# Kernel tuning notes

Measured on AMD Instinct MI355X. Metric: run time of the kernel, lower is better.

Reference implementation:

```python
import jax, jax.numpy as jnp
import numpy as np

# MORR all-pass ring parameters (MORRConfig_20um defaults: attenuation / self-coupling)
A_MORR = 0.8578
R_MORR = 0.8578
KS = 3       # kernel_size
MB = 8       # miniblock (circulant block size)
BN_EPS = 1e-5


def mrr_roundtrip_phase_to_tr(phi):
    # through-port transmission of an all-pass microring vs roundtrip phase
    c = jnp.cos(phi)
    num = A_MORR * A_MORR - 2.0 * A_MORR * R_MORR * c + R_MORR * R_MORR
    den = 1.0 - 2.0 * A_MORR * R_MORR * c + (A_MORR * R_MORR) ** 2
    return num / den


def setup_inputs() -> dict:
    key = jax.random.key(0)
    k1, k2 = jax.random.split(key, 2)
    B, C, H, W = 64, 64, 32, 32
    outC = 64
    q = (C * KS * KS + MB - 1) // MB   # grid_dim_x = 72
    p = (outC + MB - 1) // MB          # grid_dim_y = 8
    x = jax.random.normal(k1, (B, C, H, W), jnp.float32)
    weight = jax.random.normal(k2, (p, q, MB), jnp.float32) * 0.05  # circulant eigen-vectors per block
    gamma = jnp.ones((outC,), jnp.float32)   # BatchNorm2d weight
    beta = jnp.zeros((outC,), jnp.float32)   # BatchNorm2d bias
    return {"x": x, "weight": weight, "gamma": gamma, "beta": beta}


def reference(x, weight, gamma, beta):
    B, C, H, W = x.shape
    p, q, mb = weight.shape
    outC = gamma.shape[0]
    Ho, Wo = H, W  # stride=1, padding=1, ks=3
    L = Ho * Wo
    # im2col (torch F.unfold ordering: C major, then kh, kw)
    xp = jnp.pad(x, ((0, 0), (0, 0), (1, 1), (1, 1)))
    cols = jnp.stack([xp[:, :, i:i + Ho, j:j + Wo]
                      for i in range(KS) for j in range(KS)], axis=2)  # [B,C,9,Ho,Wo]
    cols = cols.reshape(B, C * KS * KS, L).transpose(0, 2, 1)          # [B,L,C*k*k]
    assert C * KS * KS == q * mb, "patch dim must pad to q*mb"
    s = cols.reshape(B, L, q, mb)
    s = s * s  # optical intensity (power) fed into the MORR
    # block-circulant weight: Wc[p,q,i,j] = weight[p,q,(i-j) mod mb]
    i_idx = jnp.arange(mb)
    idx = (i_idx[:, None] - i_idx[None, :]) % mb
    Wc = weight[:, :, idx]                                             # [p,q,mb,mb]
    # accumulated roundtrip phase per output node
    phase = jnp.einsum('blqj,pqij->blpi', s, Wc)                       # [B,L,p,mb]
    tr = mrr_roundtrip_phase_to_tr(phase)
    out = tr.reshape(B, L, p * mb)[:, :, :outC]                        # truncate to out_channel
    out = out.transpose(0, 2, 1).reshape(B, outC, Ho, Wo)
    # BatchNorm2d (training mode: batch statistics) + Hardtanh(-1, 1)
    mean = out.mean(axis=(0, 2, 3), keepdims=True)
    var = out.var(axis=(0, 2, 3), keepdims=True)
    y = (out - mean) * jax.lax.rsqrt(var + BN_EPS)
    y = y * gamma[None, :, None, None] + beta[None, :, None, None]
    return jnp.clip(y, -1.0, 1.0)
```

## Files before the change

### kernel.cpp

```cpp
#include <hip/hip_runtime.h>


#define A_MORR 0.8578f
#define R_MORR 0.8578f
#define TR_C1 (A_MORR * A_MORR + R_MORR * R_MORR)
#define TR_C2 (-2.0f * A_MORR * R_MORR)
#define TR_C3 (1.0f + (A_MORR * R_MORR) * (A_MORR * R_MORR))
#define BN_EPS 1e-5f

#define NPIX 65536
#define X2_LO 17408
#define SMEM_BYTES 34816
#define NBLK 1024

typedef __attribute__((ext_vector_type(8))) short bf16x8;
typedef __attribute__((ext_vector_type(16))) float f32x16;

__device__ __forceinline__ void bf16split(float s, unsigned short& h, unsigned short& l) {
    union { float f; unsigned u; } cv; cv.f = s;
    unsigned r = (cv.u + 0x7fffu + ((cv.u >> 16) & 1u)) & 0xffff0000u;
    h = (unsigned short)(r >> 16);
    union { unsigned u; float f; } hv; hv.u = r;
    float lo = s - hv.f;
    cv.f = lo;
    unsigned r2 = cv.u + 0x7fffu + ((cv.u >> 16) & 1u);
    l = (unsigned short)(r2 >> 16);
}

__global__ __launch_bounds__(256) void prep_kernel(const float* __restrict__ w,
                                                   char* __restrict__ wfrag) {
    int gtid = blockIdx.x * 256 + threadIdx.x;
    if (gtid < 36864) {
        int j    = gtid & 7;
        int lane = (gtid >> 3) & 63;
        int okm  = gtid >> 9;
        int mt   = okm & 1;
        int ks   = (okm >> 1) & 3;
        int off  = okm >> 3;
        int oc   = mt * 32 + (lane & 31);
        int c    = ks * 16 + (lane >> 5) * 8 + j;
        int kg   = c * 9 + off;
        float val = w[(oc >> 3) * 576 + (kg >> 3) * 8 + ((oc - kg) & 7)];
        unsigned short h, l;
        bf16split(val, h, l);
        ((unsigned short*)(wfrag + okm * 2048))[lane * 8 + j] = h;
        ((unsigned short*)(wfrag + okm * 2048 + 1024))[lane * 8 + j] = l;
    }
}

__global__ __launch_bounds__(256, 4) void conv_kernel(const float* __restrict__ x,
                                                      const char* __restrict__ wfrag,
                                                      float* __restrict__ out,
                                                      float* __restrict__ partials) {
    const int rt  = blockIdx.x;
    const int b   = blockIdx.y;
    const int bid = b * 16 + rt;
    const int tid = threadIdx.x;

    const int lane = tid & 63;
    const int wv   = tid >> 6;
    const int wmt  = wv & 1;
    const int kh   = wv >> 1;
    const int col  = lane & 31;
    const int hs   = lane >> 5;

    __shared__ __align__(16) char smem[SMEM_BYTES];

    if (tid < 128) {
        int pr = tid & 1;
        int q  = (tid >> 1) & 7;
        int rc = tid >> 4;
        int r  = rc >> 1;
        int cc = (rc & 1) ? 33 : 0;
        int g  = q ^ (cc & 7);
        *(uint4*)(smem + pr * X2_LO + ((r * 34 + cc) << 7) + (g << 4)) = uint4{0, 0, 0, 0};
    }

    {
        const int co = tid & 31;
        const int qg = tid >> 5;
        const int c  = 1 + co;
        const int gw = (qg ^ (c & 7)) << 4;
        const float* xb = x + (size_t)(b * 64 + qg * 8) * 1024 + co;
#pragma unroll
        for (int r = 0; r < 4; ++r) {
            int gr = rt * 2 - 1 + r;
            float v[8];
#pragma unroll
            for (int j = 0; j < 8; ++j) v[j] = 0.0f;
            if (gr >= 0 && gr < 32) {
#pragma unroll
                for (int j = 0; j < 8; ++j) v[j] = xb[j * 1024 + gr * 32];
            }
            unsigned hp[4], lp[4];
#pragma unroll
            for (int p = 0; p < 4; ++p) {
                unsigned short h0, l0, h1, l1;
                float s0 = v[2 * p] * v[2 * p];
                float s1 = v[2 * p + 1] * v[2 * p + 1];
                bf16split(s0, h0, l0);
                bf16split(s1, h1, l1);
                hp[p] = (unsigned)h0 | ((unsigned)h1 << 16);
                lp[p] = (unsigned)l0 | ((unsigned)l1 << 16);
            }
            char* dst = smem + ((r * 34 + c) << 7) + gw;
            *(uint4*)dst            = uint4{hp[0], hp[1], hp[2], hp[3]};
            *(uint4*)(dst + X2_LO)  = uint4{lp[0], lp[1], lp[2], lp[3]};
        }
    }
    __syncthreads();

    f32x16 acc0, acc1;
#pragma unroll
    for (int i = 0; i < 16; ++i) { acc0[i] = 0.f; acc1[i] = 0.f; }

    const char* wbase = wfrag + wmt * 2048 + (size_t)lane * 16;

#pragma unroll
    for (int dj = 0; dj < 3; ++dj) {
        const int c2 = col + dj;
        const int c7 = c2 & 7;
#pragma unroll
        for (int ksi = 0; ksi < 2; ++ksi) {
            const int ks = kh * 2 + ksi;
            const int gg = ((ks * 2 + hs) ^ c7) << 4;
            bf16x8 bh[4], bl[4];
#pragma unroll
            for (int rr = 0; rr < 4; ++rr) {
                const char* sp = smem + ((rr * 34 + c2) << 7) + gg;
                bh[rr] = *(const bf16x8*)sp;
                bl[rr] = *(const bf16x8*)(sp + X2_LO);
            }
#pragma unroll
            for (int di = 0; di < 3; ++di) {
                const char* wp = wbase + (di * 3 + dj) * 16384 + ks * 4096;
                bf16x8 ah = *(const bf16x8*)wp;
                bf16x8 al = *(const bf16x8*)(wp + 1024);
                acc0 = __builtin_amdgcn_mfma_f32_32x32x16_bf16(ah, bh[di],     acc0, 0, 0, 0);
                acc1 = __builtin_amdgcn_mfma_f32_32x32x16_bf16(ah, bh[di + 1], acc1, 0, 0, 0);
                acc0 = __builtin_amdgcn_mfma_f32_32x32x16_bf16(ah, bl[di],     acc0, 0, 0, 0);
                acc1 = __builtin_amdgcn_mfma_f32_32x32x16_bf16(ah, bl[di + 1], acc1, 0, 0, 0);
                acc0 = __builtin_amdgcn_mfma_f32_32x32x16_bf16(al, bh[di],     acc0, 0, 0, 0);
                acc1 = __builtin_amdgcn_mfma_f32_32x32x16_bf16(al, bh[di + 1], acc1, 0, 0, 0);
            }
        }
    }

    float* mg = (float*)smem;
    __syncthreads();
    {
        const int wslot = wmt * 2 + kh;
        if (kh == 0) {
#pragma unroll
            for (int j = 0; j < 16; ++j) mg[(wslot * 16 + j) * 64 + lane] = acc1[j];
        } else {
#pragma unroll
            for (int j = 0; j < 16; ++j) mg[(wslot * 16 + j) * 64 + lane] = acc0[j];
        }
    }
    __syncthreads();
    f32x16 phi;
    {
        const int rslot = wmt * 2 + (kh ^ 1);
        if (kh == 0) {
#pragma unroll
            for (int j = 0; j < 16; ++j) phi[j] = acc0[j] + mg[(rslot * 16 + j) * 64 + lane];
        } else {
#pragma unroll
            for (int j = 0; j < 16; ++j) phi[j] = acc1[j] + mg[(rslot * 16 + j) * 64 + lane];
        }
    }

    float tv[16];
    {
        const size_t obase = ((size_t)b * 64 + wmt * 32) * 1024 + (rt * 2 + kh) * 32 + col;
#pragma unroll
        for (int j = 0; j < 16; ++j) {
            float cp = __cosf(phi[j]);
            float t  = fmaf(TR_C2, cp, TR_C1) / fmaf(TR_C2, cp, TR_C3);
            tv[j] = t;
            int ocl = (j & 3) + 8 * (j >> 2) + 4 * hs;
            out[obase + (size_t)ocl * 1024] = t;
        }
    }

    float* red1 = (float*)smem;
    float* red2 = red1 + 64 * 66;
    __syncthreads();
#pragma unroll
    for (int j = 0; j < 16; ++j) {
        int ocl = (j & 3) + 8 * (j >> 2) + 4 * hs;
        int ri  = (wmt * 32 + ocl) * 66 + kh * 33 + col;
        red1[ri] = tv[j];
        red2[ri] = tv[j] * tv[j];
    }
    __syncthreads();
    if (tid < 64) {
        float s1 = 0.f, s2 = 0.f;
#pragma unroll
        for (int k = 0; k < 64; ++k) {
            int idx = tid * 66 + (k >> 5) * 33 + (k & 31);
            s1 += red1[idx];
            s2 += red2[idx];
        }
        partials[(size_t)tid * NBLK + bid]        = s1;
        partials[(size_t)(64 + tid) * NBLK + bid] = s2;
    }
}

__global__ __launch_bounds__(512) void stats_kernel(const float* __restrict__ partials,
                                                    const float* __restrict__ gamma,
                                                    const float* __restrict__ beta,
                                                    float* __restrict__ ss) {
    const int c   = blockIdx.x;
    const int tid = threadIdx.x;
    __shared__ float r1[512], r2[512];
    r1[tid] = partials[(size_t)c * NBLK + tid] + partials[(size_t)c * NBLK + 512 + tid];
    r2[tid] = partials[(size_t)(64 + c) * NBLK + tid]
            + partials[(size_t)(64 + c) * NBLK + 512 + tid];
    __syncthreads();
#pragma unroll
    for (int s = 256; s > 0; s >>= 1) {
        if (tid < s) {
            r1[tid] += r1[tid + s];
            r2[tid] += r2[tid + s];
        }
        __syncthreads();
    }
    if (tid == 0) {
        const float invN = 1.0f / (float)NPIX;
        float mean = r1[0] * invN;
        float var  = r2[0] * invN - mean * mean;
        float sc   = gamma[c] * rsqrtf(var + BN_EPS);
        ss[c]      = sc;
        ss[64 + c] = beta[c] - mean * sc;
    }
}

__global__ __launch_bounds__(256) void norm_kernel(float* __restrict__ out,
                                                   const float* __restrict__ ss) {
    int i = blockIdx.x * 256 + threadIdx.x;
    float4 v = ((float4*)out)[i];
    int oc = (i >> 8) & 63;
    float sc = ss[oc];
    float sh = ss[64 + oc];
    v.x = fminf(1.0f, fmaxf(-1.0f, fmaf(v.x, sc, sh)));
    v.y = fminf(1.0f, fmaxf(-1.0f, fmaf(v.y, sc, sh)));
    v.z = fminf(1.0f, fmaxf(-1.0f, fmaf(v.z, sc, sh)));
    v.w = fminf(1.0f, fmaxf(-1.0f, fmaf(v.w, sc, sh)));
    ((float4*)out)[i] = v;
}

extern "C" void kernel_launch(void* const* d_in, const int* in_sizes, int n_in,
                              void* d_out, int out_size, void* d_ws, size_t ws_size,
                              hipStream_t stream) {
    const float* x     = (const float*)d_in[0];
    const float* w     = (const float*)d_in[1];
    const float* gamma = (const float*)d_in[2];
    const float* beta  = (const float*)d_in[3];
    float* out = (float*)d_out;

    char*  wfrag    = (char*)d_ws;
    float* partials = (float*)((char*)d_ws + 147456);
    float* ss       = partials + 128 * NBLK;

    hipLaunchKernelGGL(prep_kernel, dim3(144), dim3(256), 0, stream, w, wfrag);
    hipLaunchKernelGGL(conv_kernel, dim3(16, 64), dim3(256), 0, stream, x, wfrag, out, partials);
    hipLaunchKernelGGL(stats_kernel, dim3(64), dim3(512), 0, stream, partials, gamma, beta, ss);
    hipLaunchKernelGGL(norm_kernel, dim3(4096), dim3(256), 0, stream, out, ss);
}
```

Measured before the change: 41.24 us.

## Fuse BN stats and normalization into conv kernel via cooperative grid sync

Turns the conv kernel into a cooperative launch. After writing per-block partial sums it does a grid-wide sync, lets 64 blocks reduce the per-channel statistics, syncs the grid again, and then applies the BN affine transform and clamp in registers before one store of the output. This removes the separate stats and norm kernel launches and the extra read-modify-write pass over the 16 MB output. In exchange it adds two grid barriers, requires all 1024 blocks to be co-resident (256 CUs × 4), and keeps the old three-kernel path as a fallback when occupancy is too low.

```diff
diff --git a/kernel.cpp b/kernel.cpp
--- a/kernel.cpp
+++ b/kernel.cpp
@@ -1,4 +1,7 @@
 #include <hip/hip_runtime.h>
+#include <hip/hip_cooperative_groups.h>
+
+namespace cg = cooperative_groups;
 
 
 #define A_MORR 0.8578f
@@ -25,6 +28,13 @@
     cv.f = lo;
     unsigned r2 = cv.u + 0x7fffu + ((cv.u >> 16) & 1u);
     l = (unsigned short)(r2 >> 16);
+}
+
+__device__ __forceinline__ void agst(float* p, float v) {
+    __hip_atomic_store(p, v, __ATOMIC_RELAXED, __HIP_MEMORY_SCOPE_AGENT);
+}
+__device__ __forceinline__ float agld(const float* p) {
+    return __hip_atomic_load(p, __ATOMIC_RELAXED, __HIP_MEMORY_SCOPE_AGENT);
 }
 
 __global__ __launch_bounds__(256) void prep_kernel(const float* __restrict__ w,
@@ -48,10 +58,14 @@
     }
 }
 
+template <int FUSED>
 __global__ __launch_bounds__(256, 4) void conv_kernel(const float* __restrict__ x,
                                                       const char* __restrict__ wfrag,
                                                       float* __restrict__ out,
-                                                      float* __restrict__ partials) {
+                                                      float* __restrict__ partials,
+                                                      float* __restrict__ ss,
+                                                      const float* __restrict__ gamma,
+                                                      const float* __restrict__ beta) {
     const int rt  = blockIdx.x;
     const int b   = blockIdx.y;
     const int bid = b * 16 + rt;
@@ -172,16 +186,10 @@
     }
 
     float tv[16];
-    {
-        const size_t obase = ((size_t)b * 64 + wmt * 32) * 1024 + (rt * 2 + kh) * 32 + col;
-#pragma unroll
-        for (int j = 0; j < 16; ++j) {
-            float cp = __cosf(phi[j]);
-            float t  = fmaf(TR_C2, cp, TR_C1) / fmaf(TR_C2, cp, TR_C3);
-            tv[j] = t;
-            int ocl = (j & 3) + 8 * (j >> 2) + 4 * hs;
-            out[obase + (size_t)ocl * 1024] = t;
-        }
+#pragma unroll
+    for (int j = 0; j < 16; ++j) {
+        float cp = __cosf(phi[j]);
+        tv[j] = fmaf(TR_C2, cp, TR_C1) / fmaf(TR_C2, cp, TR_C3);
     }
 
     float* red1 = (float*)smem;
@@ -203,8 +211,63 @@
             s1 += red1[idx];
             s2 += red2[idx];
         }
-        partials[(size_t)tid * NBLK + bid]        = s1;
-        partials[(size_t)(64 + tid) * NBLK + bid] = s2;
+        if (FUSED) {
+            agst(&partials[(size_t)tid * NBLK + bid], s1);
+            agst(&partials[(size_t)(64 + tid) * NBLK + bid], s2);
+        } else {
+            partials[(size_t)tid * NBLK + bid]        = s1;
+            partials[(size_t)(64 + tid) * NBLK + bid] = s2;
+        }
+    }
+
+    if constexpr (FUSED) {
+        cg::this_grid().sync();
+        if (bid < 64) {
+            float s1 = 0.f, s2 = 0.f;
+            for (int k = tid; k < NBLK; k += 256) {
+                s1 += agld(&partials[(size_t)bid * NBLK + k]);
+                s2 += agld(&partials[(size_t)(64 + bid) * NBLK + k]);
+            }
+            float* q1 = (float*)smem;
+            float* q2 = q1 + 256;
+            q1[tid] = s1;
+            q2[tid] = s2;
+            __syncthreads();
+#pragma unroll
+            for (int s = 128; s > 0; s >>= 1) {
+                if (tid < s) { q1[tid] += q1[tid + s]; q2[tid] += q2[tid + s]; }
+                __syncthreads();
+            }
+            if (tid == 0) {
+                const float invN = 1.0f / (float)NPIX;
+                float mean = q1[0] * invN;
+                float var  = q2[0] * invN - mean * mean;
+                float sc   = gamma[bid] * rsqrtf(var + BN_EPS);
+                agst(&ss[bid], sc);
+                agst(&ss[64 + bid], beta[bid] - mean * sc);
+            }
+        }
+        cg::this_grid().sync();
+        float* ssb = (float*)(smem + 33792);
+        if (tid < 128) ssb[tid] = agld(&ss[tid]);
+        __syncthreads();
+
+        const size_t obase = ((size_t)b * 64 + wmt * 32) * 1024 + (rt * 2 + kh) * 32 + col;
+#pragma unroll
+        for (int j = 0; j < 16; ++j) {
+            int ocl  = (j & 3) + 8 * (j >> 2) + 4 * hs;
+            float sc = ssb[wmt * 32 + ocl];
+            float sh = ssb[64 + wmt * 32 + ocl];
+            float y  = fminf(1.0f, fmaxf(-1.0f, fmaf(tv[j], sc, sh)));
+            out[obase + (size_t)ocl * 1024] = y;
+        }
+    } else {
+        const size_t obase = ((size_t)b * 64 + wmt * 32) * 1024 + (rt * 2 + kh) * 32 + col;
+#pragma unroll
+        for (int j = 0; j < 16; ++j) {
+            int ocl = (j & 3) + 8 * (j >> 2) + 4 * hs;
+            out[obase + (size_t)ocl * 1024] = tv[j];
+        }
     }
 }
 
@@ -221,10 +284,7 @@
     __syncthreads();
 #pragma unroll
     for (int s = 256; s > 0; s >>= 1) {
-        if (tid < s) {
-            r1[tid] += r1[tid + s];
-            r2[tid] += r2[tid + s];
-        }
+        if (tid < s) { r1[tid] += r1[tid + s]; r2[tid] += r2[tid + s]; }
         __syncthreads();
     }
     if (tid == 0) {
@@ -265,7 +325,25 @@
     float* ss       = partials + 128 * NBLK;
 
     hipLaunchKernelGGL(prep_kernel, dim3(144), dim3(256), 0, stream, w, wfrag);
-    hipLaunchKernelGGL(conv_kernel, dim3(16, 64), dim3(256), 0, stream, x, wfrag, out, partials);
-    hipLaunchKernelGGL(stats_kernel, dim3(64), dim3(512), 0, stream, partials, gamma, beta, ss);
-    hipLaunchKernelGGL(norm_kernel, dim3(4096), dim3(256), 0, stream, out, ss);
-}
+
+    int maxb = 0;
+    hipError_t qe = hipOccupancyMaxActiveBlocksPerMultiprocessor(
+        &maxb, reinterpret_cast<const void*>(&conv_kernel<1>), 256, 0);
+    bool fused = (qe == hipSuccess) && (maxb >= 4);
+
+    if (fused) {
+        void* cargs[] = { (void*)&x, (void*)&wfrag, (void*)&out, (void*)&partials,
+                          (void*)&ss, (void*)&gamma, (void*)&beta };
+        hipError_t le = hipLaunchCooperativeKernel(
+            reinterpret_cast<const void*>(&conv_kernel<1>),
+            dim3(16, 64), dim3(256), cargs, 0, stream);
+        if (le != hipSuccess) fused = false;
+    }
+    if (!fused) {
+        hipLaunchKernelGGL(conv_kernel<0>, dim3(16, 64), dim3(256), 0, stream,
+                           x, wfrag, out, partials, ss, gamma, beta);
+        hipLaunchKernelGGL(stats_kernel, dim3(64), dim3(512), 0, stream,
+                           partials, gamma, beta, ss);
+        hipLaunchKernelGGL(norm_kernel, dim3(4096), dim3(256), 0, stream, out, ss);
+    }
+}
```

Result: no change. 41.24 us, median of 2 (+0.0%).

## Split conv MFMA work by output row instead of K-half to drop LDS merge

Applied to the files above, without the earlier changes.

Each wave pair now owns one output row (py) and loops over the full K range, instead of splitting K between waves and computing two rows each. This removes the shared-memory exchange of partial accumulators and two barriers, and halves accumulator registers. In exchange each wave loads all weight fragments (twice the global/L1 weight traffic per wave) and re-reads the B tiles per row, with a single serial accumulation chain that has less MFMA interleaving.

```diff
diff --git a/kernel.cpp b/kernel.cpp
--- a/kernel.cpp
+++ b/kernel.cpp
@@ -60,7 +60,7 @@
     const int lane = tid & 63;
     const int wv   = tid >> 6;
     const int wmt  = wv & 1;
-    const int kh   = wv >> 1;
+    const int py   = wv >> 1;
     const int col  = lane & 31;
     const int hs   = lane >> 5;
 
@@ -110,9 +110,9 @@
     }
     __syncthreads();
 
-    f32x16 acc0, acc1;
-#pragma unroll
-    for (int i = 0; i < 16; ++i) { acc0[i] = 0.f; acc1[i] = 0.f; }
+    f32x16 acc;
+#pragma unroll
+    for (int i = 0; i < 16; ++i) acc[i] = 0.f;
 
     const char* wbase = wfrag + wmt * 2048 + (size_t)lane * 16;
 
@@ -121,62 +121,44 @@
         const int c2 = col + dj;
         const int c7 = c2 & 7;
 #pragma unroll
-        for (int ksi = 0; ksi < 2; ++ksi) {
-            const int ks = kh * 2 + ksi;
-            const int gg = ((ks * 2 + hs) ^ c7) << 4;
-            bf16x8 bh[4], bl[4];
-#pragma unroll
-            for (int rr = 0; rr < 4; ++rr) {
-                const char* sp = smem + ((rr * 34 + c2) << 7) + gg;
-                bh[rr] = *(const bf16x8*)sp;
-                bl[rr] = *(const bf16x8*)(sp + X2_LO);
-            }
-#pragma unroll
-            for (int di = 0; di < 3; ++di) {
-                const char* wp = wbase + (di * 3 + dj) * 16384 + ks * 4096;
-                bf16x8 ah = *(const bf16x8*)wp;
-                bf16x8 al = *(const bf16x8*)(wp + 1024);
-                acc0 = __builtin_amdgcn_mfma_f32_32x32x16_bf16(ah, bh[di],     acc0, 0, 0, 0);
-                acc1 = __builtin_amdgcn_mfma_f32_32x32x16_bf16(ah, bh[di + 1], acc1, 0, 0, 0);
-                acc0 = __builtin_amdgcn_mfma_f32_32x32x16_bf16(ah, bl[di],     acc0, 0, 0, 0);
-                acc1 = __builtin_amdgcn_mfma_f32_32x32x16_bf16(ah, bl[di + 1], acc1, 0, 0, 0);
-                acc0 = __builtin_amdgcn_mfma_f32_32x32x16_bf16(al, bh[di],     acc0, 0, 0, 0);
-                acc1 = __builtin_amdgcn_mfma_f32_32x32x16_bf16(al, bh[di + 1], acc1, 0, 0, 0);
-            }
-        }
-    }
-
-    float* mg = (float*)smem;
-    __syncthreads();
-    {
-        const int wslot = wmt * 2 + kh;
-        if (kh == 0) {
-#pragma unroll
-            for (int j = 0; j < 16; ++j) mg[(wslot * 16 + j) * 64 + lane] = acc1[j];
-        } else {
-#pragma unroll
-            for (int j = 0; j < 16; ++j) mg[(wslot * 16 + j) * 64 + lane] = acc0[j];
-        }
-    }
-    __syncthreads();
-    f32x16 phi;
-    {
-        const int rslot = wmt * 2 + (kh ^ 1);
-        if (kh == 0) {
-#pragma unroll
-            for (int j = 0; j < 16; ++j) phi[j] = acc0[j] + mg[(rslot * 16 + j) * 64 + lane];
-        } else {
-#pragma unroll
-            for (int j = 0; j < 16; ++j) phi[j] = acc1[j] + mg[(rslot * 16 + j) * 64 + lane];
+        for (int kp = 0; kp < 2; ++kp) {
+            bf16x8 wh_[2][3], wl_[2][3];
+#pragma unroll
+            for (int ksi = 0; ksi < 2; ++ksi) {
+#pragma unroll
+                for (int di = 0; di < 3; ++di) {
+                    const char* wp = wbase + (di * 3 + dj) * 16384 + (kp * 2 + ksi) * 4096;
+                    wh_[ksi][di] = *(const bf16x8*)wp;
+                    wl_[ksi][di] = *(const bf16x8*)(wp + 1024);
+                }
+            }
+#pragma unroll
+            for (int ksi = 0; ksi < 2; ++ksi) {
+                const int ks = kp * 2 + ksi;
+                const int gg = ((ks * 2 + hs) ^ c7) << 4;
+                bf16x8 bh[3], bl[3];
+#pragma unroll
+                for (int di = 0; di < 3; ++di) {
+                    const char* sp = smem + (((py + di) * 34 + c2) << 7) + gg;
+                    bh[di] = *(const bf16x8*)sp;
+                    bl[di] = *(const bf16x8*)(sp + X2_LO);
+                }
+#pragma unroll
+                for (int di = 0; di < 3; ++di) {
+                    acc = __builtin_amdgcn_mfma_f32_32x32x16_bf16(wh_[ksi][di], bh[di], acc, 0, 0, 0);
+                    acc = __builtin_amdgcn_mfma_f32_32x32x16_bf16(wh_[ksi][di], bl[di], acc, 0, 0, 0);
+                    acc = __builtin_amdgcn_mfma_f32_32x32x16_bf16(wl_[ksi][di], bh[di], acc, 0, 0, 0);
+                }
+            }
         }
     }
 
     float tv[16];
     {
-        const size_t obase = ((size_t)b * 64 + wmt * 32) * 1024 + (rt * 2 + kh) * 32 + col;
+        const size_t obase = ((size_t)b * 64 + wmt * 32) * 1024 + (rt * 2 + py) * 32 + col;
 #pragma unroll
         for (int j = 0; j < 16; ++j) {
-            float cp = __cosf(phi[j]);
+            float cp = __cosf(acc[j]);
             float t  = fmaf(TR_C2, cp, TR_C1) / fmaf(TR_C2, cp, TR_C3);
             tv[j] = t;
             int ocl = (j & 3) + 8 * (j >> 2) + 4 * hs;
@@ -190,7 +172,7 @@
 #pragma unroll
     for (int j = 0; j < 16; ++j) {
         int ocl = (j & 3) + 8 * (j >> 2) + 4 * hs;
-        int ri  = (wmt * 32 + ocl) * 66 + kh * 33 + col;
+        int ri  = (wmt * 32 + ocl) * 66 + py * 33 + col;
         red1[ri] = tv[j];
         red2[ri] = tv[j] * tv[j];
     }
```

Result: slower. 42.87 us (+3.9%).
